# Kernel optimization log

Hardware: AMD Instinct MI355X
Metric: run time of the kernel (lower is better)

Reference implementation:

```python
import jax, jax.numpy as jnp
import numpy as np

H = 768; B = 8; T = 1024; V = 50257
S = 256      # token_distribution_samples
K = 64       # token_topk
POOL = 1024  # max(S*4, K) token pool
TEMP = 0.1; LIM = 0.25; MW = 0.1


def _ln(x, g, b):
    m = x.mean(-1, keepdims=True)
    v = ((x - m) ** 2).mean(-1, keepdims=True)
    return (x - m) / jnp.sqrt(v + 1e-5) * g + b


def _head(x, g, b, w1, b1, w2, b2):
    # LayerNorm -> Linear -> GELU(exact) -> (Dropout=identity in eval) -> Linear
    h = _ln(x, g, b) @ w1 + b1
    h = jax.nn.gelu(h, approximate=False)
    return h @ w2 + b2


def _l2norm(x):
    return x / jnp.maximum(jnp.linalg.norm(x, axis=-1, keepdims=True), 1e-12)


def setup_inputs() -> dict:
    key = jax.random.key(0)
    ks = jax.random.split(key, 16)
    init = lambda k, shp: jax.random.normal(k, shp, jnp.float32) * 0.02
    f32 = jnp.float32
    return {
        "latent": jax.random.normal(ks[0], (B, T, H), f32),
        "token_embedding_matrix": jax.random.normal(ks[1], (V, H), f32),
        # scale head
        "scale_ln_g": jnp.ones((H,), f32), "scale_ln_b": jnp.zeros((H,), f32),
        "scale_w1": init(ks[2], (H, H)), "scale_b1": jnp.zeros((H,), f32),
        "scale_w2": init(ks[3], (H, H)), "scale_b2": jnp.zeros((H,), f32),
        # bias head
        "bias_ln_g": jnp.ones((H,), f32), "bias_ln_b": jnp.zeros((H,), f32),
        "bias_w1": init(ks[4], (H, H)), "bias_b1": jnp.zeros((H,), f32),
        "bias_w2": init(ks[5], (H, H)), "bias_b2": jnp.zeros((H,), f32),
        # contrastive head (projection_dim == H)
        "con_ln_g": jnp.ones((H,), f32), "con_ln_b": jnp.zeros((H,), f32),
        "con_w1": init(ks[6], (H, H)), "con_b1": jnp.zeros((H,), f32),
        "con_w2": init(ks[7], (H, H)), "con_b2": jnp.zeros((H,), f32),
        # deterministic augmentation noise (randn_like * 0.01)
        "noise_a": jax.random.normal(ks[8], (B * T, H), f32) * 0.01,
        "noise_b": jax.random.normal(ks[9], (B * T, H), f32) * 0.01,
        # deterministic row-sampling (torch.randperm analogues)
        "samp_idx": jax.random.permutation(ks[10], B * T)[:S].astype(jnp.int32),
        "tok_idx": jax.random.permutation(ks[11], V)[:POOL].astype(jnp.int32),
    }


def reference(latent, token_embedding_matrix,
              scale_ln_g, scale_ln_b, scale_w1, scale_b1, scale_w2, scale_b2,
              bias_ln_g, bias_ln_b, bias_w1, bias_b1, bias_w2, bias_b2,
              con_ln_g, con_ln_b, con_w1, con_b1, con_w2, con_b2,
              noise_a, noise_b, samp_idx, tok_idx):
    # compensate: u = s(z)*z + b(z)
    scale = 1.0 + LIM * jnp.tanh(_head(latent, scale_ln_g, scale_ln_b, scale_w1, scale_b1, scale_w2, scale_b2))
    bias = LIM * jnp.tanh(_head(latent, bias_ln_g, bias_ln_b, bias_w1, bias_b1, bias_w2, bias_b2))
    aligned = scale * latent + bias

    flat = aligned.reshape(-1, H)  # [N, H], N = B*T
    # contrastive loss
    va = _l2norm(_head(flat + noise_a, con_ln_g, con_ln_b, con_w1, con_b1, con_w2, con_b2))
    vb = _l2norm(_head(flat + noise_b, con_ln_g, con_ln_b, con_w1, con_b1, con_w2, con_b2))
    logits = va @ vb.T / TEMP  # [N, N]
    loss_ab = -jnp.mean(jnp.diagonal(jax.nn.log_softmax(logits, axis=-1)))
    loss_ba = -jnp.mean(jnp.diagonal(jax.nn.log_softmax(logits.T, axis=-1)))
    con_loss = 0.5 * (loss_ab + loss_ba)

    # token distribution loss
    af = flat[samp_idx]                     # [S, H]
    te = token_embedding_matrix[tok_idx]    # [POOL, H]
    tl = _l2norm(af) @ _l2norm(te).T / TEMP  # [S, POOL]
    top_vals, top_idx = jax.lax.top_k(tl, K)
    top_emb = te[top_idx]                   # [S, K, H] gather
    w = jax.nn.softmax(top_vals, axis=-1)[..., None]
    proto = (w * top_emb).sum(axis=1)       # [S, H]
    proto_loss = jnp.mean((af - proto) ** 2)
    moment_loss = jnp.mean((af.mean(0) - te.mean(0)) ** 2) \
        + jnp.mean((af.std(0) - te.std(0)) ** 2)
    token_dist_loss = proto_loss + MW * moment_loss

    comp_reg_loss = jnp.mean((scale - 1.0) ** 2) + jnp.mean(bias ** 2)
    return (aligned, con_loss, token_dist_loss, comp_reg_loss, scale, bias)
```

## Files before the change

### kernel.cpp

```cpp
#include <hip/hip_runtime.h>
#include <hip/hip_bf16.h>

typedef __hip_bfloat16 bf16;
typedef __attribute__((ext_vector_type(4))) float f32x4;
typedef __attribute__((ext_vector_type(8))) short bf16x8v;

static constexpr int   HD    = 768;
static constexpr int   NRr   = 8192;
static constexpr int   SSAMP = 256;
static constexpr int   KTOP  = 64;
static constexpr int   NPOOL = 1024;
static constexpr float TINV  = 10.0f;

__device__ __forceinline__ float bf2f(bf16 h){ return __bfloat162float(h); }
__device__ __forceinline__ bf16  f2bf(float f){ return __float2bfloat16(f); }

__device__ __forceinline__ float gelu_exact(float x){
  return 0.5f * x * (1.0f + erff(x * 0.70710678118654752f));
}

__device__ __forceinline__ float block_sum(float v, float* buf){
  const int lane = threadIdx.x & 63, w = threadIdx.x >> 6;
  const int nw = (int)blockDim.x >> 6;
  #pragma unroll
  for(int o = 32; o; o >>= 1) v += __shfl_down(v, o);
  __syncthreads();
  if(lane == 0) buf[w] = v;
  __syncthreads();
  float t = 0.f;
  for(int i = 0; i < nw; i++) t += buf[i];
  return t;
}

__device__ __forceinline__ void block_sum2(float& a, float& b, float* buf){
  const int lane = threadIdx.x & 63, w = threadIdx.x >> 6;
  #pragma unroll
  for(int o = 32; o; o >>= 1){ a += __shfl_down(a, o); b += __shfl_down(b, o); }
  __syncthreads();
  if(lane == 0){ buf[w] = a; buf[4 + w] = b; }
  __syncthreads();
  float ta = 0.f, tb = 0.f;
  #pragma unroll
  for(int i = 0; i < 4; i++){ ta += buf[i]; tb += buf[4 + i]; }
  a = ta; b = tb;
}

__device__ __forceinline__ void gload_lds16(const bf16* g, bf16* lds_uniform){
  __builtin_amdgcn_global_load_lds(
      (const __attribute__((address_space(1))) unsigned int*)(const void*)g,
      (__attribute__((address_space(3))) unsigned int*)(void*)lds_uniform,
      16, 0, 0);
}

struct TsA { const float* w[6]; const float* gg[6]; bf16* o[6]; };
__global__ __launch_bounds__(256)
void tscale6(TsA a){
  __shared__ float t[32][33];
  const int z = blockIdx.z;
  const float* Win = a.w[z];
  const float* g   = a.gg[z];
  bf16* Wt         = a.o[z];
  const int tx = threadIdx.x, ty = threadIdx.y;
  const int bx = blockIdx.x * 32, by = blockIdx.y * 32;
  #pragma unroll
  for(int j = 0; j < 4; j++)
    t[ty + j*8][tx] = Win[(size_t)(by + ty + j*8) * HD + bx + tx];
  __syncthreads();
  const float gv = g ? g[by + tx] : 1.0f;
  #pragma unroll
  for(int j = 0; j < 4; j++)
    Wt[(size_t)(bx + ty + j*8) * HD + by + tx] = f2bf(gv * t[tx][ty + j*8]);
}

struct FbA { const float* bln[3]; const float* w1[3]; const float* b1[3]; float* o[3]; };
__global__ __launch_bounds__(256)
void foldbias3(FbA a){
  __shared__ float red[4][64];
  const int h = blockIdx.y;
  const int lane = threadIdx.x & 63, w = threadIdx.x >> 6;
  const int n = blockIdx.x * 64 + lane;
  const float* bl = a.bln[h];
  const float* w1 = a.w1[h];
  float t = 0.f;
  for(int k = w * 192; k < w * 192 + 192; k++)
    t += bl[k] * w1[(size_t)k * HD + n];
  red[w][lane] = t;
  __syncthreads();
  if(w == 0)
    a.o[h][n] = a.b1[h][n] + red[0][lane] + red[1][lane] + red[2][lane] + red[3][lane];
}

__global__ __launch_bounds__(256)
void lnxh_kernel(const float* __restrict__ x, bf16* __restrict__ o){
  __shared__ float buf[4];
  const int row = blockIdx.x, tid = threadIdx.x;
  const size_t base = (size_t)row * HD;
  float v[3];
  #pragma unroll
  for(int j = 0; j < 3; j++) v[j] = x[base + tid + j*256];
  float s = v[0] + v[1] + v[2];
  s = block_sum(s, buf);
  const float m = s * (1.0f / HD);
  float q = 0.f;
  #pragma unroll
  for(int j = 0; j < 3; j++){ const float d = v[j] - m; q += d*d; }
  q = block_sum(q, buf);
  const float inv = rsqrtf(q * (1.0f / HD) + 1e-5f);
  #pragma unroll
  for(int j = 0; j < 3; j++)
    o[base + tid + j*256] = f2bf((v[j] - m) * inv);
}

__global__ __launch_bounds__(256)
void fuse_al_ln(const float* __restrict__ latent, const float* __restrict__ sc,
                const float* __restrict__ bi, const float* __restrict__ na,
                const float* __restrict__ nb, float* __restrict__ out_aligned,
                bf16* __restrict__ X){
  __shared__ float buf[8];
  const int row = blockIdx.x, tid = threadIdx.x;
  const size_t base = (size_t)row * HD;
  float ua[3], ub[3];
  #pragma unroll
  for(int j = 0; j < 3; j++){
    const int i = tid + j*256;
    const float a = sc[base + i] * latent[base + i] + bi[base + i];
    out_aligned[base + i] = a;
    ua[j] = a + na[base + i];
    ub[j] = a + nb[base + i];
  }
  float sa = ua[0] + ua[1] + ua[2];
  float sb = ub[0] + ub[1] + ub[2];
  block_sum2(sa, sb, buf);
  const float ma = sa * (1.0f / HD), mb = sb * (1.0f / HD);
  float qa = 0.f, qb = 0.f;
  #pragma unroll
  for(int j = 0; j < 3; j++){
    const float da = ua[j] - ma; qa += da*da;
    const float db = ub[j] - mb; qb += db*db;
  }
  block_sum2(qa, qb, buf);
  const float ia = rsqrtf(qa * (1.0f / HD) + 1e-5f);
  const float ib = rsqrtf(qb * (1.0f / HD) + 1e-5f);
  #pragma unroll
  for(int j = 0; j < 3; j++){
    const int i = tid + j*256;
    X[base + i] = f2bf((ua[j] - ma) * ia);
    X[(size_t)(row + NRr) * HD + i] = f2bf((ub[j] - mb) * ib);
  }
}

enum { EPI_GELU = 0, EPI_SB = 1, EPI_RAW = 3, EPI_LOGITS = 4 };

template<int EPI>
__global__ __launch_bounds__(256, 2)
void gemm_kernel(const bf16* __restrict__ A, const bf16* __restrict__ Bt,
                 const bf16* __restrict__ Bt2,
                 const int M, const int N, const int K,
                 const int lda, const int ldc,
                 const float* __restrict__ bias, const float* __restrict__ bias2,
                 bf16* __restrict__ outb, float* __restrict__ outf,
                 float* __restrict__ outf2,
                 float* __restrict__ aux, float* __restrict__ aux2){
  __shared__ __align__(16) bf16 As[128 * 64];
  __shared__ __align__(16) bf16 Bs[128 * 64];
  __shared__ float rbuf[512];

  const int tid  = threadIdx.x;
  const int wave = tid >> 6, lane = tid & 63;
  const int wm = wave >> 1, wn = wave & 1;
  const int r16 = lane & 15, kh = lane >> 4;
  const int bx = blockIdx.x, by = blockIdx.y;
  const int row0 = by * 128, col0 = bx * 128;

  float addv = 0.f;
  if constexpr(EPI == EPI_SB){
    if(blockIdx.z == 0){ addv = 1.0f; }
    else { A += 768; Bt = Bt2; bias = bias2; outf = outf2; }
  }

  f32x4 acc[4][4];
  #pragma unroll
  for(int i = 0; i < 4; i++)
    #pragma unroll
    for(int j = 0; j < 4; j++){ f32x4 z = {0.f,0.f,0.f,0.f}; acc[i][j] = z; }

  const bf16* gA[4]; const bf16* gB[4];
  bf16* lA[4]; bf16* lB[4];
  #pragma unroll
  for(int j = 0; j < 4; j++){
    const int c = tid + j*256;
    const int rr = c >> 3, p = c & 7;
    const int g = (p - (rr & 7)) & 7;
    gA[j] = A  + (size_t)(row0 + rr) * lda + g * 8;
    gB[j] = Bt + (size_t)(col0 + rr) * K   + g * 8;
    lA[j] = As + ((size_t)j*256 + wave*64) * 8;
    lB[j] = Bs + ((size_t)j*256 + wave*64) * 8;
  }
  const int sw = r16 & 7;

  for(int k0 = 0; k0 < K; k0 += 64){
    __syncthreads();
    #pragma unroll
    for(int j = 0; j < 4; j++){
      gload_lds16(gA[j] + k0, lA[j]);
      gload_lds16(gB[j] + k0, lB[j]);
    }
    __syncthreads();
    #pragma unroll
    for(int kk = 0; kk < 2; kk++){
      const int koff = ((kk*4 + kh + sw) & 7) * 8;
      bf16x8v av[4], bv[4];
      #pragma unroll
      for(int f = 0; f < 4; f++){
        av[f] = *(const bf16x8v*)(As + (wm*64 + f*16 + r16) * 64 + koff);
        bv[f] = *(const bf16x8v*)(Bs + (wn*64 + f*16 + r16) * 64 + koff);
      }
      #pragma unroll
      for(int i = 0; i < 4; i++)
        #pragma unroll
        for(int j = 0; j < 4; j++)
          acc[i][j] = __builtin_amdgcn_mfma_f32_16x16x32_bf16(av[i], bv[j], acc[i][j], 0, 0, 0);
    }
  }

  const int crow0 = row0 + wm * 64;
  const int ccol0 = col0 + wn * 64;

  if constexpr(EPI != EPI_LOGITS){
    float part = 0.f;
    #pragma unroll
    for(int i = 0; i < 4; i++){
      #pragma unroll
      for(int j = 0; j < 4; j++){
        const int col = ccol0 + j*16 + r16;
        const float bvv = bias ? bias[col] : 0.f;
        #pragma unroll
        for(int q = 0; q < 4; q++){
          const int row = crow0 + i*16 + kh*4 + q;
          const float v = acc[i][j][q] + bvv;
          const size_t off = (size_t)row * ldc + col;
          if constexpr(EPI == EPI_GELU){
            outb[off] = f2bf(gelu_exact(v));
          } else if constexpr(EPI == EPI_SB){
            const float t = 0.25f * tanhf(v);
            outf[off] = t + addv;
            part += t * t;
          } else {
            outb[off] = f2bf(v);
          }
        }
      }
    }
    if constexpr(EPI == EPI_SB){
      const float tot2 = block_sum(part, rbuf);
      if(tid == 0)
        aux[(size_t)blockIdx.z * (gridDim.x * gridDim.y) + by * gridDim.x + bx] = tot2;
    }
  } else {
    float rs[16], cs[4];
    #pragma unroll
    for(int t = 0; t < 16; t++) rs[t] = 0.f;
    #pragma unroll
    for(int t = 0; t < 4; t++) cs[t] = 0.f;
    #pragma unroll
    for(int i = 0; i < 4; i++)
      #pragma unroll
      for(int j = 0; j < 4; j++)
        #pragma unroll
        for(int q = 0; q < 4; q++){
          const float ev = expf(acc[i][j][q] * TINV);
          rs[i*4 + q] += ev;
          cs[j]       += ev;
        }
    #pragma unroll
    for(int t = 0; t < 16; t++){
      float r = rs[t];
      r += __shfl_xor(r, 1); r += __shfl_xor(r, 2);
      r += __shfl_xor(r, 4); r += __shfl_xor(r, 8);
      rs[t] = r;
    }
    if(r16 == 0){
      #pragma unroll
      for(int i = 0; i < 4; i++)
        #pragma unroll
        for(int q = 0; q < 4; q++)
          rbuf[wn*128 + wm*64 + i*16 + kh*4 + q] = rs[i*4 + q];
    }
    #pragma unroll
    for(int j = 0; j < 4; j++){
      float c = cs[j];
      c += __shfl_xor(c, 16); c += __shfl_xor(c, 32);
      cs[j] = c;
    }
    if(kh == 0){
      #pragma unroll
      for(int j = 0; j < 4; j++)
        rbuf[256 + wm*128 + wn*64 + j*16 + r16] = cs[j];
    }
    __syncthreads();
    if(tid < 128){
      aux [(size_t)bx * M + row0 + tid] = rbuf[tid]       + rbuf[128 + tid];
      aux2[(size_t)by * M + col0 + tid] = rbuf[256 + tid] + rbuf[384 + tid];
    }
  }
}

__global__ __launch_bounds__(256)
void l2ndiag_kernel(bf16* __restrict__ vab, float* __restrict__ diag){
  __shared__ float buf[8];
  const int row = blockIdx.x, tid = threadIdx.x;
  const size_t basea = (size_t)row * HD;
  const size_t baseb = basea + (size_t)NRr * HD;
  float a[3], b[3];
  #pragma unroll
  for(int j = 0; j < 3; j++){
    a[j] = bf2f(vab[basea + tid + j*256]);
    b[j] = bf2f(vab[baseb + tid + j*256]);
  }
  float qa = a[0]*a[0] + a[1]*a[1] + a[2]*a[2];
  float qb = b[0]*b[0] + b[1]*b[1] + b[2]*b[2];
  block_sum2(qa, qb, buf);
  const float ia = 1.0f / fmaxf(sqrtf(qa), 1e-12f);
  const float ib = 1.0f / fmaxf(sqrtf(qb), 1e-12f);
  float d = 0.f;
  #pragma unroll
  for(int j = 0; j < 3; j++){
    const bf16 oa = f2bf(a[j] * ia);
    const bf16 ob = f2bf(b[j] * ib);
    vab[basea + tid + j*256] = oa;
    vab[baseb + tid + j*256] = ob;
    d += bf2f(oa) * bf2f(ob);
  }
  d = block_sum(d, buf);
  if(tid == 0) diag[row] = d * TINV;
}

__global__ __launch_bounds__(256)
void rcsum_kernel(const float* __restrict__ rp, const float* __restrict__ cp,
                  float* __restrict__ rs, float* __restrict__ cs, const int nb){
  const int i = blockIdx.x * 256 + threadIdx.x;
  float r = 0.f, c = 0.f;
  for(int b = 0; b < nb; b++){
    r += rp[(size_t)b * NRr + i];
    c += cp[(size_t)b * NRr + i];
  }
  rs[i] = r; cs[i] = c;
}

__global__ __launch_bounds__(256)
void gather_kernel(const float* __restrict__ aligned, const int* __restrict__ samp,
                   float* __restrict__ afraw, bf16* __restrict__ afn,
                   const float* __restrict__ emb, const int* __restrict__ tok,
                   float* __restrict__ teg, bf16* __restrict__ ten){
  __shared__ float buf[4];
  const int tid = threadIdx.x;
  if(blockIdx.x < SSAMP){
    const int s = blockIdx.x;
    const size_t src = (size_t)samp[s] * HD, dst = (size_t)s * HD;
    float v[3];
    #pragma unroll
    for(int j = 0; j < 3; j++){
      const int i = tid + j*256;
      v[j] = aligned[src + i];
      afraw[dst + i] = v[j];
    }
    float q = v[0]*v[0] + v[1]*v[1] + v[2]*v[2];
    q = block_sum(q, buf);
    const float inv = 1.0f / fmaxf(sqrtf(q), 1e-12f);
    #pragma unroll
    for(int j = 0; j < 3; j++) afn[dst + tid + j*256] = f2bf(v[j] * inv);
  } else {
    const int p = blockIdx.x - SSAMP;
    const size_t src = (size_t)tok[p] * HD, dst = (size_t)p * HD;
    float v[3];
    #pragma unroll
    for(int j = 0; j < 3; j++){
      const int i = tid + j*256;
      v[j] = emb[src + i];
      teg[dst + i] = v[j];
    }
    float q = v[0]*v[0] + v[1]*v[1] + v[2]*v[2];
    q = block_sum(q, buf);
    const float inv = 1.0f / fmaxf(sqrtf(q), 1e-12f);
    #pragma unroll
    for(int j = 0; j < 3; j++) ten[dst + tid + j*256] = f2bf(v[j] * inv);
  }
}

__global__ __launch_bounds__(256)
void topk_kernel(const bf16* __restrict__ afn, const bf16* __restrict__ ten,
                 const float* __restrict__ teg, const float* __restrict__ afraw,
                 float* __restrict__ protopart){
  __shared__ float saf[HD];
  __shared__ float sv[NPOOL];
  __shared__ float topv[KTOP];
  __shared__ int   topi[KTOP];
  __shared__ float wts[KTOP];
  __shared__ float rv[4];
  __shared__ int   ri[4];
  __shared__ float buf[4];
  __shared__ float sinv;
  const int s = blockIdx.x, tid = threadIdx.x;
  const int lane = tid & 63, w = tid >> 6;
  #pragma unroll
  for(int j = 0; j < 3; j++) saf[tid + j*256] = bf2f(afn[(size_t)s * HD + tid + j*256]);
  __syncthreads();
  #pragma unroll
  for(int cb = 0; cb < 4; cb++){
    const int c = tid + cb * 256;
    const bf16* tr = ten + (size_t)c * HD;
    float d = 0.f;
    for(int k = 0; k < HD; k += 8){
      int4 rawv = *(const int4*)(tr + k);
      const bf16* e = (const bf16*)&rawv;
      #pragma unroll
      for(int u = 0; u < 8; u++) d += bf2f(e[u]) * saf[k + u];
    }
    sv[c] = d * TINV;
  }
  __syncthreads();
  for(int k = 0; k < KTOP; k++){
    float bvv = -1e30f; int bi = 0x7fffffff;
    #pragma unroll
    for(int j = 0; j < 4; j++){
      const int i = tid + j*256;
      const float x = sv[i];
      if(x > bvv || (x == bvv && i < bi)){ bvv = x; bi = i; }
    }
    #pragma unroll
    for(int o = 1; o < 64; o <<= 1){
      const float ov = __shfl_xor(bvv, o);
      const int   oi = __shfl_xor(bi, o);
      if(ov > bvv || (ov == bvv && oi < bi)){ bvv = ov; bi = oi; }
    }
    if(lane == 0){ rv[w] = bvv; ri[w] = bi; }
    __syncthreads();
    if(tid == 0){
      for(int w2 = 1; w2 < 4; w2++)
        if(rv[w2] > bvv || (rv[w2] == bvv && ri[w2] < bi)){ bvv = rv[w2]; bi = ri[w2]; }
      if(bi < 0 || bi >= NPOOL) bi = 0;
      topv[k] = bvv; topi[k] = bi; sv[bi] = -1e30f;
    }
    __syncthreads();
  }
  if(tid < KTOP) wts[tid] = expf(topv[tid] - topv[0]);
  __syncthreads();
  if(tid == 0){
    float t = 0.f;
    for(int k = 0; k < KTOP; k++) t += wts[k];
    sinv = 1.0f / t;
  }
  __syncthreads();
  float part = 0.f;
  #pragma unroll
  for(int j = 0; j < 3; j++){
    const int h = tid + j*256;
    float ph = 0.f;
    for(int k = 0; k < KTOP; k++) ph += wts[k] * teg[(size_t)topi[k] * HD + h];
    ph *= sinv;
    const float d = afraw[(size_t)s * HD + h] - ph;
    part += d * d;
  }
  part = block_sum(part, buf);
  if(tid == 0) protopart[s] = part;
}

__global__ __launch_bounds__(768)
void mom1_kernel(const float* __restrict__ afraw, const float* __restrict__ teg,
                 float* __restrict__ partial){
  const int b = blockIdx.x, h = threadIdx.x;
  float sa = 0.f, sa2 = 0.f, st = 0.f, st2 = 0.f;
  for(int r = b * 40; r < b * 40 + 40; r++){
    if(r < SSAMP){
      const float v = afraw[(size_t)r * HD + h];
      sa += v; sa2 += v * v;
    } else {
      const float v = teg[(size_t)(r - SSAMP) * HD + h];
      st += v; st2 += v * v;
    }
  }
  partial[(size_t)(b*4 + 0) * HD + h] = sa;
  partial[(size_t)(b*4 + 1) * HD + h] = sa2;
  partial[(size_t)(b*4 + 2) * HD + h] = st;
  partial[(size_t)(b*4 + 3) * HD + h] = st2;
}

__global__ __launch_bounds__(1024)
void final_kernel(const float* __restrict__ rs, const float* __restrict__ cs,
                  const float* __restrict__ diag,
                  const float* __restrict__ aux, const int naux,
                  const float* __restrict__ protopart,
                  const float* __restrict__ mompart,
                  float* __restrict__ outsc){
  __shared__ float buf[16];
  const int tid = threadIdx.x;
  float s1 = 0.f, s2 = 0.f;
  for(int r = tid; r < NRr; r += 1024){
    const float dg = diag[r];
    s1 += logf(rs[r]) - dg;
    s2 += logf(cs[r]) - dg;
  }
  float c1 = 0.f;
  for(int j = tid; j < naux; j += 1024) c1 += aux[j];
  float pp = 0.f;
  for(int j = tid; j < SSAMP; j += 1024) pp += protopart[j];
  float t1p = 0.f, t2p = 0.f;
  if(tid < HD){
    float sa = 0.f, sa2 = 0.f, st = 0.f, st2 = 0.f;
    for(int b = 0; b < 32; b++){
      sa  += mompart[(size_t)(b*4 + 0) * HD + tid];
      sa2 += mompart[(size_t)(b*4 + 1) * HD + tid];
      st  += mompart[(size_t)(b*4 + 2) * HD + tid];
      st2 += mompart[(size_t)(b*4 + 3) * HD + tid];
    }
    const float ma  = sa * (1.0f / SSAMP);
    const float sda = sqrtf(fmaxf(sa2 * (1.0f / SSAMP) - ma * ma, 0.f));
    const float mt  = st * (1.0f / NPOOL);
    const float sdt = sqrtf(fmaxf(st2 * (1.0f / NPOOL) - mt * mt, 0.f));
    const float dmu = ma - mt, dsd = sda - sdt;
    t1p = dmu * dmu; t2p = dsd * dsd;
  }
  s1 = block_sum(s1, buf);
  s2 = block_sum(s2, buf);
  c1 = block_sum(c1, buf);
  pp = block_sum(pp, buf);
  const float t1 = block_sum(t1p, buf);
  const float t2 = block_sum(t2p, buf);
  if(tid == 0){
    const float con  = 0.5f * (s1 + s2) / (float)NRr;
    const float creg = c1 / 6291456.0f;
    const float tdl  = pp / (float)(SSAMP * HD) + 0.1f * ((t1 + t2) / (float)HD);
    outsc[0] = con;
    outsc[1] = tdl;
    outsc[2] = creg;
  }
}

extern "C" void kernel_launch(void* const* d_in, const int* in_sizes, int n_in,
                              void* d_out, int out_size, void* d_ws, size_t ws_size,
                              hipStream_t stream){
  (void)in_sizes; (void)n_in; (void)out_size; (void)ws_size;
  const float* latent = (const float*)d_in[0];
  const float* tokemb = (const float*)d_in[1];
  const float* s_g  = (const float*)d_in[2];  const float* s_bln = (const float*)d_in[3];
  const float* s_w1 = (const float*)d_in[4];  const float* s_b1  = (const float*)d_in[5];
  const float* s_w2 = (const float*)d_in[6];  const float* s_b2  = (const float*)d_in[7];
  const float* b_g  = (const float*)d_in[8];  const float* b_bln = (const float*)d_in[9];
  const float* b_w1 = (const float*)d_in[10]; const float* b_b1  = (const float*)d_in[11];
  const float* b_w2 = (const float*)d_in[12]; const float* b_b2  = (const float*)d_in[13];
  const float* c_g  = (const float*)d_in[14]; const float* c_bln = (const float*)d_in[15];
  const float* c_w1 = (const float*)d_in[16]; const float* c_b1  = (const float*)d_in[17];
  const float* c_w2 = (const float*)d_in[18]; const float* c_b2  = (const float*)d_in[19];
  const float* noise_a = (const float*)d_in[20];
  const float* noise_b = (const float*)d_in[21];
  const int*  samp = (const int*)d_in[22];
  const int*  tok  = (const int*)d_in[23];

  float* out = (float*)d_out;
  float* out_aligned = out;
  float* out_scalars = out + (size_t)NRr * HD;
  float* out_scale   = out + (size_t)NRr * HD + 3;
  float* out_bias    = out_scale + (size_t)NRr * HD;

  char* wp = (char*)d_ws;
  auto alloc = [&](size_t bytes) -> char* {
    char* p = wp; wp += (bytes + 255) & ~(size_t)255; return p;
  };
  bf16* wt_comb1 = (bf16*)alloc((size_t)2*HD*HD*2);
  bf16* wt_c1    = (bf16*)alloc((size_t)HD*HD*2);
  bf16* wt_s2    = (bf16*)alloc((size_t)HD*HD*2);
  bf16* wt_b2    = (bf16*)alloc((size_t)HD*HD*2);
  bf16* wt_c2    = (bf16*)alloc((size_t)HD*HD*2);
  float* bcomb1  = (float*)alloc(2*HD*4);
  float* bc1     = (float*)alloc(HD*4);
  bf16* A1 = (bf16*)alloc((size_t)2*NRr*HD*2);
  bf16* A2 = (bf16*)alloc((size_t)2*NRr*HD*2);
  float* rowpart = (float*)alloc((size_t)64*NRr*4);
  float* colpart = (float*)alloc((size_t)64*NRr*4);
  float* rowsum  = (float*)alloc((size_t)NRr*4);
  float* colsum  = (float*)alloc((size_t)NRr*4);
  float* diag    = (float*)alloc((size_t)NRr*4);
  float* aux     = (float*)alloc(768*4);
  float* afraw   = (float*)alloc((size_t)SSAMP*HD*4);
  float* teg     = (float*)alloc((size_t)NPOOL*HD*4);
  float* protopart = (float*)alloc(SSAMP*4);
  float* mompart = rowpart;
  bf16*  ten     = (bf16*)colpart;
  bf16*  afn     = (bf16*)(colpart + ((size_t)NPOOL*HD*2)/4);

  TsA ts;
  ts.w[0]=s_w1; ts.gg[0]=s_g;     ts.o[0]=wt_comb1;
  ts.w[1]=b_w1; ts.gg[1]=b_g;     ts.o[1]=wt_comb1 + (size_t)HD*HD;
  ts.w[2]=c_w1; ts.gg[2]=c_g;     ts.o[2]=wt_c1;
  ts.w[3]=s_w2; ts.gg[3]=nullptr; ts.o[3]=wt_s2;
  ts.w[4]=b_w2; ts.gg[4]=nullptr; ts.o[4]=wt_b2;
  ts.w[5]=c_w2; ts.gg[5]=nullptr; ts.o[5]=wt_c2;
  tscale6<<<dim3(24,24,6), dim3(32,8), 0, stream>>>(ts);
  FbA fb;
  fb.bln[0]=s_bln; fb.w1[0]=s_w1; fb.b1[0]=s_b1; fb.o[0]=bcomb1;
  fb.bln[1]=b_bln; fb.w1[1]=b_w1; fb.b1[1]=b_b1; fb.o[1]=bcomb1 + HD;
  fb.bln[2]=c_bln; fb.w1[2]=c_w1; fb.b1[2]=c_b1; fb.o[2]=bc1;
  foldbias3<<<dim3(12,3), 256, 0, stream>>>(fb);

  lnxh_kernel<<<NRr, 256, 0, stream>>>(latent, A2);
  gemm_kernel<EPI_GELU><<<dim3(12,64), 256, 0, stream>>>(
      A2, wt_comb1, nullptr, NRr, 2*HD, HD, HD, 2*HD, bcomb1, nullptr,
      A1, nullptr, nullptr, nullptr, nullptr);
  gemm_kernel<EPI_SB><<<dim3(6,64,2), 256, 0, stream>>>(
      A1, wt_s2, wt_b2, NRr, HD, HD, 2*HD, HD, s_b2, b_b2,
      nullptr, out_scale, out_bias, aux, nullptr);

  fuse_al_ln<<<NRr, 256, 0, stream>>>(latent, out_scale, out_bias,
                                      noise_a, noise_b, out_aligned, A1);

  gemm_kernel<EPI_GELU><<<dim3(6,128), 256, 0, stream>>>(
      A1, wt_c1, nullptr, 2*NRr, HD, HD, HD, HD, bc1, nullptr,
      A2, nullptr, nullptr, nullptr, nullptr);
  gemm_kernel<EPI_RAW><<<dim3(6,128), 256, 0, stream>>>(
      A2, wt_c2, nullptr, 2*NRr, HD, HD, HD, HD, c_b2, nullptr,
      A1, nullptr, nullptr, nullptr, nullptr);
  l2ndiag_kernel<<<NRr, 256, 0, stream>>>(A1, diag);
  bf16* va = A1;
  bf16* vb = A1 + (size_t)NRr * HD;

  gemm_kernel<EPI_LOGITS><<<dim3(64,64), 256, 0, stream>>>(
      va, vb, nullptr, NRr, NRr, HD, HD, 0, nullptr, nullptr,
      nullptr, nullptr, nullptr, rowpart, colpart);
  rcsum_kernel<<<NRr / 256, 256, 0, stream>>>(rowpart, colpart, rowsum, colsum, 64);

  gather_kernel<<<SSAMP + NPOOL, 256, 0, stream>>>(out_aligned, samp, afraw, afn,
                                                   tokemb, tok, teg, ten);
  topk_kernel<<<SSAMP, 256, 0, stream>>>(afn, ten, teg, afraw, protopart);
  mom1_kernel<<<32, 768, 0, stream>>>(afraw, teg, mompart);

  final_kernel<<<1, 1024, 0, stream>>>(rowsum, colsum, diag, aux, 768,
                                       protopart, mompart, out_scalars);
}
```

Baseline: 518.5 us.

## Replace iterative argmax top-k with shared-memory bitonic sort of pool scores

Replaces the 64-round argmax selection (each round with two block barriers and a wave shuffle reduction) with a full bitonic sort of the 1024 scores and their indices in shared memory, then takes the first 64 entries. The intent is to cut the long serial chain of barriers and single-thread steps in the top-k phase. In exchange the sort runs 55 barrier-separated compare-exchange stages over the whole pool, and shared-memory use grows by an index array. Tie-breaking prefers the lower index, as the old code did.

```diff
diff --git a/kernel.cpp b/kernel.cpp
--- a/kernel.cpp
+++ b/kernel.cpp
@@ -393,15 +393,11 @@
                  float* __restrict__ protopart){
   __shared__ float saf[HD];
   __shared__ float sv[NPOOL];
-  __shared__ float topv[KTOP];
-  __shared__ int   topi[KTOP];
+  __shared__ int   si[NPOOL];
   __shared__ float wts[KTOP];
-  __shared__ float rv[4];
-  __shared__ int   ri[4];
   __shared__ float buf[4];
   __shared__ float sinv;
   const int s = blockIdx.x, tid = threadIdx.x;
-  const int lane = tid & 63, w = tid >> 6;
   #pragma unroll
   for(int j = 0; j < 3; j++) saf[tid + j*256] = bf2f(afn[(size_t)s * HD + tid + j*256]);
   __syncthreads();
@@ -417,33 +413,27 @@
       for(int u = 0; u < 8; u++) d += bf2f(e[u]) * saf[k + u];
     }
     sv[c] = d * TINV;
-  }
-  __syncthreads();
-  for(int k = 0; k < KTOP; k++){
-    float bvv = -1e30f; int bi = 0x7fffffff;
-    #pragma unroll
-    for(int j = 0; j < 4; j++){
-      const int i = tid + j*256;
-      const float x = sv[i];
-      if(x > bvv || (x == bvv && i < bi)){ bvv = x; bi = i; }
-    }
-    #pragma unroll
-    for(int o = 1; o < 64; o <<= 1){
-      const float ov = __shfl_xor(bvv, o);
-      const int   oi = __shfl_xor(bi, o);
-      if(ov > bvv || (ov == bvv && oi < bi)){ bvv = ov; bi = oi; }
-    }
-    if(lane == 0){ rv[w] = bvv; ri[w] = bi; }
-    __syncthreads();
-    if(tid == 0){
-      for(int w2 = 1; w2 < 4; w2++)
-        if(rv[w2] > bvv || (rv[w2] == bvv && ri[w2] < bi)){ bvv = rv[w2]; bi = ri[w2]; }
-      if(bi < 0 || bi >= NPOOL) bi = 0;
-      topv[k] = bvv; topi[k] = bi; sv[bi] = -1e30f;
-    }
-    __syncthreads();
-  }
-  if(tid < KTOP) wts[tid] = expf(topv[tid] - topv[0]);
+    si[c] = c;
+  }
+  for(int k2 = 2; k2 <= NPOOL; k2 <<= 1){
+    for(int j = k2 >> 1; j > 0; j >>= 1){
+      __syncthreads();
+      #pragma unroll
+      for(int q = 0; q < 4; q++){
+        const int i = tid + q * 256;
+        const int ixj = i ^ j;
+        if(ixj > i){
+          const float v1 = sv[i],  v2 = sv[ixj];
+          const int   i1 = si[i],  i2 = si[ixj];
+          const bool g = (v1 > v2) || (v1 == v2 && i1 < i2);
+          const bool swap = ((i & k2) == 0) ? !g : g;
+          if(swap){ sv[i] = v2; sv[ixj] = v1; si[i] = i2; si[ixj] = i1; }
+        }
+      }
+    }
+  }
+  __syncthreads();
+  if(tid < KTOP) wts[tid] = expf(sv[tid] - sv[0]);
   __syncthreads();
   if(tid == 0){
     float t = 0.f;
@@ -456,7 +446,7 @@
   for(int j = 0; j < 3; j++){
     const int h = tid + j*256;
     float ph = 0.f;
-    for(int k = 0; k < KTOP; k++) ph += wts[k] * teg[(size_t)topi[k] * HD + h];
+    for(int k = 0; k < KTOP; k++) ph += wts[k] * teg[(size_t)si[k] * HD + h];
     ph *= sinv;
     const float d = afraw[(size_t)s * HD + h] - ph;
     part += d * d;
```

Measured after the change: 481.2 us. 7.2% less time.
